# Kernel optimization log

Measured on AMD Instinct MI355X. Metric: run time of the kernel, lower is better.

The kernel has to match this reference:

```python
import jax, jax.numpy as jnp
import numpy as np

B, D = 65536, 365

def _linp(k, fan_in, fan_out):
    # torch nn.Linear default init: U(-1/sqrt(fan_in), 1/sqrt(fan_in))
    kw, kb = jax.random.split(k)
    bound = 1.0 / np.sqrt(fan_in)
    W = jax.random.uniform(kw, (fan_in, fan_out), jnp.float32, -bound, bound)
    b = jax.random.uniform(kb, (fan_out,), jnp.float32, -bound, bound)
    return W, b

def setup_inputs() -> dict:
    key = jax.random.key(0)
    ks = jax.random.split(key, 9)
    x = jax.random.normal(ks[0], (B, D), jnp.float32)
    W1, b1 = _linp(ks[1], D, 512)
    W2, b2 = _linp(ks[2], 512, 256)
    W3, b3 = _linp(ks[3], 256, 128)
    Ws, bs = _linp(ks[4], 6, 32)
    Wc1, bc1 = _linp(ks[5], 128 + 32, 64)
    Wc2, bc2 = _linp(ks[6], 64, 32)
    Wc3, bc3 = _linp(ks[7], 32, 1)
    return dict(x=x, W1=W1, b1=b1, W2=W2, b2=b2, W3=W3, b3=b3,
                Ws=Ws, bs=bs, Wc1=Wc1, bc1=bc1, Wc2=Wc2, bc2=bc2,
                Wc3=Wc3, bc3=bc3)

def _row_stats(x):
    # fused row-wise moments: mean, std (ddof=1), min, max, skew, kurtosis
    mu = jnp.mean(x, axis=1, keepdims=True)          # [B,1]
    c = x - mu                                        # [B,D]
    var1 = jnp.sum(c * c, axis=1) / (x.shape[1] - 1)  # unbiased, matches torch.std()
    sigma = jnp.sqrt(var1)
    m3 = jnp.mean(c ** 3, axis=1)
    m4 = jnp.mean(c ** 4, axis=1)
    skew = m3 / (sigma ** 3 + 1e-8)
    kurt = m4 / (sigma ** 4 + 1e-8)
    return jnp.stack([mu[:, 0], sigma, jnp.min(x, axis=1), jnp.max(x, axis=1), skew, kurt], axis=1)

def reference(x, W1, b1, W2, b2, W3, b3, Ws, bs, Wc1, bc1, Wc2, bc2, Wc3, bc3):
    h = jax.nn.relu(x @ W1 + b1)
    h = jax.nn.relu(h @ W2 + b2)
    seq = jax.nn.relu(h @ W3 + b3)            # [B,128]
    stat = _row_stats(x) @ Ws + bs            # [B,32]
    comb = jnp.concatenate([seq, stat], axis=1)
    c = jax.nn.relu(comb @ Wc1 + bc1)
    c = jax.nn.relu(c @ Wc2 + bc2)
    out = jax.nn.sigmoid(c @ Wc3 + bc3)       # [B,1]
    return out[:, 0]
```

## Files before the change

### kernel.cpp

```cpp
#include <hip/hip_runtime.h>
#include <math.h>

typedef __attribute__((ext_vector_type(8)))  short short8;
typedef __attribute__((ext_vector_type(16))) float float16;

#define DEVI __device__ __forceinline__

DEVI short f2bf(float f) {
    unsigned u = __float_as_uint(f);
    u = (u + 0x7fffu + ((u >> 16) & 1u)) >> 16;
    return (short)u;
}
DEVI unsigned pk2(float a, float b) {
    return (unsigned)(unsigned short)f2bf(a) | ((unsigned)(unsigned short)f2bf(b) << 16);
}
DEVI float16 mfma16(short8 a, short8 b, float16 c) {
    return __builtin_amdgcn_mfma_f32_32x32x16_bf16(a, b, c, 0, 0, 0);
}
DEVI int rowof(int r, int h) { return (r & 3) + 8 * (r >> 2) + 4 * h; }
DEVI short8 lds8(const short* p) { return *(const short8*)p; }

#define W1T_OFF  0
#define W2T_OFF  188416
#define W3T_OFF  319488
#define WC1T_OFF 352256
#define WC2T_OFF 362496

__global__ void prep_v2(const float* __restrict__ W1, const float* __restrict__ W2,
                        const float* __restrict__ W3, const float* __restrict__ Wc1,
                        const float* __restrict__ Wc2, short* __restrict__ ws) {
    __shared__ short T[16 * 72];
    int b = blockIdx.x, t = threadIdx.x;
    const float* src; int K, N; size_t base; int kc, nb;
    if (b < 184)        {            src = W1;  K = 365; N = 512; base = W1T_OFF;  kc = b >> 3;  nb = b & 7; }
    else if (b < 312)   { int l = b - 184; src = W2;  K = 512; N = 256; base = W2T_OFF;  kc = l >> 2;  nb = l & 3; }
    else if (b < 344)   { int l = b - 312; src = W3;  K = 256; N = 128; base = W3T_OFF;  kc = l >> 1;  nb = l & 1; }
    else if (b < 354)   {            src = Wc1; K = 160; N = 64;  base = WC1T_OFF; kc = b - 344; nb = 0; }
    else                {            src = Wc2; K = 64;  N = 32;  base = WC2T_OFF; kc = b - 354; nb = 0; }
    int n = nb * 64 + (t & 63);
    int kr = t >> 6;
    #pragma unroll
    for (int i = 0; i < 4; ++i) {
        int krow = kr + 4 * i;
        int k = kc * 16 + krow;
        float v = (k < K && n < N) ? src[(size_t)k * N + n] : 0.f;
        T[krow * 72 + (t & 63)] = f2bf(v);
    }
    __syncthreads();
    int n2 = t >> 2, ksq = (t & 3) * 4;
    int ng = nb * 64 + n2;
    if (ng < N) {
        unsigned lo = (unsigned)(unsigned short)T[ksq * 72 + n2]
                    | ((unsigned)(unsigned short)T[(ksq + 1) * 72 + n2] << 16);
        unsigned hi = (unsigned)(unsigned short)T[(ksq + 2) * 72 + n2]
                    | ((unsigned)(unsigned short)T[(ksq + 3) * 72 + n2] << 16);
        uint2 d; d.x = lo; d.y = hi;
        *(uint2*)(ws + base + ((size_t)kc * N + ng) * 16 + ksq) = d;
    }
}

__global__ __launch_bounds__(512, 4)
void fused_v2(const float* __restrict__ x,
              const float* __restrict__ b1f, const float* __restrict__ b2f,
              const float* __restrict__ b3f, const float* __restrict__ Wsf,
              const float* __restrict__ bsf, const float* __restrict__ bc1f,
              const float* __restrict__ bc2f, const float* __restrict__ Wc3f,
              const float* __restrict__ bc3f,
              const short* __restrict__ wsw, float* __restrict__ out)
{
    __shared__ __align__(16) char smem[65536];
    short* XT    = (short*)smem;
    short* SB    = (short*)(smem + 48128);
    short* C1    = (short*)smem;
    short* FEATL = (short*)(smem + 12288);
    float* C2    = (float*)(smem + 20480);

    const short* W1t  = wsw + W1T_OFF;
    const short* W2t  = wsw + W2T_OFF;
    const short* W3t  = wsw + W3T_OFF;
    const short* Wc1t = wsw + WC1T_OFF;
    const short* Wc2t = wsw + WC2T_OFF;

    const int tid  = (int)threadIdx.x;
    const int lane = tid & 63;
    const int wv   = tid >> 6;
    const int m    = lane & 31;
    const int h    = lane >> 5;
    const int mt   = wv & 1;
    const int nl   = wv >> 1;
    const int rowBase = (int)blockIdx.x * 64;

    const int r0 = tid >> 3, j0 = tid & 7;
    const float* xrow = x + (size_t)(rowBase + r0) * 365;
    float s1 = 0.f, s2 = 0.f, s3 = 0.f, s4 = 0.f, mn = 1e30f, mx = -1e30f;
    #pragma unroll
    for (int i = 0; i < 6; ++i) {
        int o = j0 + 8 * i;
        if (o <= 45) {
            float xf[8];
            #pragma unroll
            for (int jj = 0; jj < 8; ++jj) {
                int col = o * 8 + jj;
                xf[jj] = (col < 365) ? xrow[col] : 0.f;
            }
            #pragma unroll
            for (int jj = 0; jj < 8; ++jj) {
                int col = o * 8 + jj;
                if (col < 365) {
                    float v = xf[jj], v2 = v * v;
                    s1 += v; s2 += v2; s3 += v2 * v; s4 += v2 * v2;
                    mn = fminf(mn, v); mx = fmaxf(mx, v);
                }
            }
            int4 w4;
            w4.x = (int)pk2(xf[0], xf[1]); w4.y = (int)pk2(xf[2], xf[3]);
            w4.z = (int)pk2(xf[4], xf[5]); w4.w = (int)pk2(xf[6], xf[7]);
            *(int4*)(XT + r0 * 376 + o * 8) = w4;
        }
    }
    #pragma unroll
    for (int off = 1; off <= 4; off <<= 1) {
        s1 += __shfl_xor(s1, off); s2 += __shfl_xor(s2, off);
        s3 += __shfl_xor(s3, off); s4 += __shfl_xor(s4, off);
        mn = fminf(mn, __shfl_xor(mn, off)); mx = fmaxf(mx, __shfl_xor(mx, off));
    }
    unsigned fdw0, fdw1;
    {
        float mean  = s1 * (1.0f / 365.0f);
        float var1  = (s2 - 365.0f * mean * mean) * (1.0f / 364.0f);
        float sigma = sqrtf(var1);
        float m3 = (s3 - 3.0f * mean * s2) * (1.0f / 365.0f) + 2.0f * mean * mean * mean;
        float mm = mean * mean;
        float m4 = (s4 - 4.0f * mean * s3 + 6.0f * mm * s2) * (1.0f / 365.0f) - 3.0f * mm * mm;
        float sg2 = sigma * sigma;
        float skew = m3 / (sigma * sg2 + 1e-8f);
        float kurt = m4 / (sg2 * sg2 + 1e-8f);
        float st[6] = { mean, sigma, mn, mx, skew, kurt };
        float f[4];
        #pragma unroll
        for (int c0 = 0; c0 < 4; ++c0) {
            int c = 4 * j0 + c0;
            float acc = bsf[c];
            #pragma unroll
            for (int jj = 0; jj < 6; ++jj) acc += st[jj] * Wsf[jj * 32 + c];
            f[c0] = acc;
        }
        fdw0 = pk2(f[0], f[1]); fdw1 = pk2(f[2], f[3]);
    }
    __syncthreads();

    float16 h2a0, h2a1;
    #pragma unroll
    for (int i = 0; i < 16; ++i) { h2a0[i] = 0.f; h2a1[i] = 0.f; }

    const short* Ap = XT + (mt * 32 + m) * 376 + h * 8;

    for (int p = 0; p < 2; ++p) {
        float16 ga0, ga1;
        #pragma unroll
        for (int i = 0; i < 16; ++i) { ga0[i] = 0.f; ga1[i] = 0.f; }
        int nc0 = 256 * p + 32 * nl;
        const short* Bp0 = W1t + (nc0 + m) * 16 + h * 8;
        const short* Bp1 = Bp0 + 128 * 16;
        #pragma unroll
        for (int kc = 0; kc < 23; ++kc) {
            short8 a  = lds8(Ap + kc * 16);
            short8 b0 = *(const short8*)(Bp0 + kc * 8192);
            short8 b1 = *(const short8*)(Bp1 + kc * 8192);
            ga0 = mfma16(a, b0, ga0);
            ga1 = mfma16(a, b1, ga1);
        }
        #pragma unroll
        for (int q = 0; q < 2; ++q) {
            __syncthreads();
            {
                int nc = 256 * p + 128 * q + 32 * nl;
                float bb = b1f[nc + m];
                float16 A;
                if (q) A = ga1; else A = ga0;
                #pragma unroll
                for (int r = 0; r < 16; ++r) {
                    int rw = mt * 32 + rowof(r, h);
                    SB[rw * 136 + 32 * nl + m] = f2bf(fmaxf(A[r] + bb, 0.f));
                }
            }
            __syncthreads();
            int slab = 2 * p + q;
            const short* A2p  = SB + (mt * 32 + m) * 136 + h * 8;
            const short* B2p0 = W2t + (size_t)slab * 8 * 4096 + (32 * nl + m) * 16 + h * 8;
            const short* B2p1 = B2p0 + 128 * 16;
            #pragma unroll
            for (int i = 0; i < 8; ++i) {
                short8 a  = lds8(A2p + i * 16);
                short8 b0 = *(const short8*)(B2p0 + i * 4096);
                short8 b1 = *(const short8*)(B2p1 + i * 4096);
                h2a0 = mfma16(a, b0, h2a0);
                h2a1 = mfma16(a, b1, h2a1);
            }
        }
    }

    float16 g3a;
    #pragma unroll
    for (int i = 0; i < 16; ++i) g3a[i] = 0.f;
    for (int s = 0; s < 2; ++s) {
        __syncthreads();
        {
            float bb = b2f[32 * nl + 128 * s + m];
            float16 A;
            if (s) A = h2a1; else A = h2a0;
            #pragma unroll
            for (int r = 0; r < 16; ++r) {
                int rw = mt * 32 + rowof(r, h);
                SB[rw * 136 + 32 * nl + m] = f2bf(fmaxf(A[r] + bb, 0.f));
            }
        }
        __syncthreads();
        const short* A3p = SB + (mt * 32 + m) * 136 + h * 8;
        const short* B3p = W3t + (size_t)s * 8 * 2048 + (32 * nl + m) * 16 + h * 8;
        #pragma unroll
        for (int i = 0; i < 8; ++i) {
            short8 a = lds8(A3p + i * 16);
            short8 b = *(const short8*)(B3p + i * 2048);
            g3a = mfma16(a, b, g3a);
        }
    }

    __syncthreads();
    {
        float bb = b3f[32 * nl + m];
        #pragma unroll
        for (int r = 0; r < 16; ++r) {
            int rw = mt * 32 + rowof(r, h);
            SB[rw * 136 + 32 * nl + m] = f2bf(fmaxf(g3a[r] + bb, 0.f));
        }
        *(unsigned*)(FEATL + r0 * 40 + 4 * j0)     = fdw0;
        *(unsigned*)(FEATL + r0 * 40 + 4 * j0 + 2) = fdw1;
    }
    __syncthreads();

    if (wv < 4) {
        int nt4 = wv >> 1;
        float16 g4a;
        #pragma unroll
        for (int i = 0; i < 16; ++i) g4a[i] = 0.f;
        const short* A4p = SB + (mt * 32 + m) * 136 + h * 8;
        const short* B4p = Wc1t + (32 * nt4 + m) * 16 + h * 8;
        #pragma unroll
        for (int i = 0; i < 8; ++i) {
            short8 a = lds8(A4p + i * 16);
            short8 b = *(const short8*)(B4p + i * 1024);
            g4a = mfma16(a, b, g4a);
        }
        const short* AF = FEATL + (mt * 32 + m) * 40 + h * 8;
        #pragma unroll
        for (int i = 0; i < 2; ++i) {
            short8 a = lds8(AF + i * 16);
            short8 b = *(const short8*)(B4p + (8 + i) * 1024);
            g4a = mfma16(a, b, g4a);
        }
        float bb = bc1f[32 * nt4 + m];
        #pragma unroll
        for (int r = 0; r < 16; ++r) {
            int rw = mt * 32 + rowof(r, h);
            C1[rw * 72 + 32 * nt4 + m] = f2bf(fmaxf(g4a[r] + bb, 0.f));
        }
    }
    __syncthreads();

    if (wv < 2) {
        float16 g5;
        #pragma unroll
        for (int i = 0; i < 16; ++i) g5[i] = 0.f;
        const short* A5p = C1 + (wv * 32 + m) * 72 + h * 8;
        const short* B5p = Wc2t + m * 16 + h * 8;
        #pragma unroll
        for (int i = 0; i < 4; ++i) {
            short8 a = lds8(A5p + i * 16);
            short8 b = *(const short8*)(B5p + i * 512);
            g5 = mfma16(a, b, g5);
        }
        float bb = bc2f[m];
        #pragma unroll
        for (int r = 0; r < 16; ++r) {
            int rw = wv * 32 + rowof(r, h);
            C2[rw * 33 + m] = fmaxf(g5[r] + bb, 0.f);
        }
    }
    __syncthreads();

    if (tid < 64) {
        float z = bc3f[0];
        #pragma unroll
        for (int i = 0; i < 32; ++i) z += C2[tid * 33 + i] * Wc3f[i];
        out[rowBase + tid] = 1.0f / (1.0f + expf(-z));
    }
}

extern "C" void kernel_launch(void* const* d_in, const int* in_sizes, int n_in,
                              void* d_out, int out_size, void* d_ws, size_t ws_size,
                              hipStream_t stream)
{
    (void)in_sizes; (void)n_in; (void)out_size; (void)ws_size;
    const float* x   = (const float*)d_in[0];
    const float* W1  = (const float*)d_in[1];
    const float* b1  = (const float*)d_in[2];
    const float* W2  = (const float*)d_in[3];
    const float* b2  = (const float*)d_in[4];
    const float* W3  = (const float*)d_in[5];
    const float* b3  = (const float*)d_in[6];
    const float* Ws  = (const float*)d_in[7];
    const float* bs  = (const float*)d_in[8];
    const float* Wc1 = (const float*)d_in[9];
    const float* bc1 = (const float*)d_in[10];
    const float* Wc2 = (const float*)d_in[11];
    const float* bc2 = (const float*)d_in[12];
    const float* Wc3 = (const float*)d_in[13];
    const float* bc3 = (const float*)d_in[14];
    short* ws = (short*)d_ws;

    prep_v2<<<358, 256, 0, stream>>>(W1, W2, W3, Wc1, Wc2, ws);
    fused_v2<<<1024, 512, 0, stream>>>(x, b1, b2, b3, Ws, bs, bc1, bc2, Wc3, bc3,
                                       ws, (float*)d_out);
}
```

Measured before the change: 237.5 us.

## Software-prefetch weight fragments through register ring buffers and restructure layer-1 loop

Weight B-fragments for every MLP layer are now loaded from global memory a few steps ahead into small register ring buffers, so global load latency overlaps with MFMA work instead of stalling each iteration. The layer-1 loop is reorganized into four 128-wide column passes with one accumulator each, interleaving layer-2 accumulation after every pass. Biases are hoisted into registers at kernel start, and x loads and output stores use nontemporal hints. The added prefetch registers may raise register pressure and risk occupancy loss under the 512x4 launch bounds.

```diff
diff --git a/kernel.cpp b/kernel.cpp
--- a/kernel.cpp
+++ b/kernel.cpp
@@ -19,6 +19,7 @@
 }
 DEVI int rowof(int r, int h) { return (r & 3) + 8 * (r >> 2) + 4 * h; }
 DEVI short8 lds8(const short* p) { return *(const short8*)p; }
+DEVI short8 gld8(const short* p) { return *(const short8*)p; }
 
 #define W1T_OFF  0
 #define W2T_OFF  188416
@@ -60,7 +61,7 @@
 }
 
 __global__ __launch_bounds__(512, 4)
-void fused_v2(const float* __restrict__ x,
+void fused_v3(const float* __restrict__ x,
               const float* __restrict__ b1f, const float* __restrict__ b2f,
               const float* __restrict__ b3f, const float* __restrict__ Wsf,
               const float* __restrict__ bsf, const float* __restrict__ bc1f,
@@ -87,8 +88,22 @@
     const int m    = lane & 31;
     const int h    = lane >> 5;
     const int mt   = wv & 1;
-    const int nl   = wv >> 1;
+    const int nc   = wv >> 1;
     const int rowBase = (int)blockIdx.x * 64;
+
+    const short* B1b  = W1t + (nc * 32 + m) * 16 + h * 8;
+    const short* B2b0 = W2t + (nc * 32 + m) * 16 + h * 8;
+    const short* B2b1 = B2b0 + 128 * 16;
+    short8 rb[4], rc0[2], rc1[2];
+    #pragma unroll
+    for (int i = 0; i < 4; ++i) rb[i] = gld8(B1b + i * 8192);
+    #pragma unroll
+    for (int i = 0; i < 2; ++i) { rc0[i] = gld8(B2b0 + i * 4096); rc1[i] = gld8(B2b1 + i * 4096); }
+    float bb1[4];
+    #pragma unroll
+    for (int p = 0; p < 4; ++p) bb1[p] = b1f[p * 128 + nc * 32 + m];
+    float bb2a = b2f[nc * 32 + m], bb2b = b2f[128 + nc * 32 + m];
+    float bb3 = b3f[nc * 32 + m];
 
     const int r0 = tid >> 3, j0 = tid & 7;
     const float* xrow = x + (size_t)(rowBase + r0) * 365;
@@ -101,7 +116,7 @@
             #pragma unroll
             for (int jj = 0; jj < 8; ++jj) {
                 int col = o * 8 + jj;
-                xf[jj] = (col < 365) ? xrow[col] : 0.f;
+                xf[jj] = (col < 365) ? __builtin_nontemporal_load(xrow + col) : 0.f;
             }
             #pragma unroll
             for (int jj = 0; jj < 8; ++jj) {
@@ -152,88 +167,83 @@
     float16 h2a0, h2a1;
     #pragma unroll
     for (int i = 0; i < 16; ++i) { h2a0[i] = 0.f; h2a1[i] = 0.f; }
-
-    const short* Ap = XT + (mt * 32 + m) * 376 + h * 8;
-
-    for (int p = 0; p < 2; ++p) {
-        float16 ga0, ga1;
-        #pragma unroll
-        for (int i = 0; i < 16; ++i) { ga0[i] = 0.f; ga1[i] = 0.f; }
-        int nc0 = 256 * p + 32 * nl;
-        const short* Bp0 = W1t + (nc0 + m) * 16 + h * 8;
-        const short* Bp1 = Bp0 + 128 * 16;
+    const short* Ap  = XT + (mt * 32 + m) * 376 + h * 8;
+    const short* A2p = SB + (mt * 32 + m) * 136 + h * 8;
+
+    #pragma unroll
+    for (int p = 0; p < 4; ++p) {
+        float16 ga;
+        #pragma unroll
+        for (int i = 0; i < 16; ++i) ga[i] = 0.f;
         #pragma unroll
         for (int kc = 0; kc < 23; ++kc) {
-            short8 a  = lds8(Ap + kc * 16);
-            short8 b0 = *(const short8*)(Bp0 + kc * 8192);
-            short8 b1 = *(const short8*)(Bp1 + kc * 8192);
-            ga0 = mfma16(a, b0, ga0);
-            ga1 = mfma16(a, b1, ga1);
-        }
-        #pragma unroll
-        for (int q = 0; q < 2; ++q) {
-            __syncthreads();
-            {
-                int nc = 256 * p + 128 * q + 32 * nl;
-                float bb = b1f[nc + m];
-                float16 A;
-                if (q) A = ga1; else A = ga0;
-                #pragma unroll
-                for (int r = 0; r < 16; ++r) {
-                    int rw = mt * 32 + rowof(r, h);
-                    SB[rw * 136 + 32 * nl + m] = f2bf(fmaxf(A[r] + bb, 0.f));
-                }
+            int t = p * 23 + kc;
+            short8 b = rb[t & 3];
+            int tn = t + 4;
+            if (tn < 92) {
+                int pp = tn / 23, kk = tn - pp * 23;
+                rb[tn & 3] = gld8(B1b + pp * 2048 + kk * 8192);
             }
-            __syncthreads();
-            int slab = 2 * p + q;
-            const short* A2p  = SB + (mt * 32 + m) * 136 + h * 8;
-            const short* B2p0 = W2t + (size_t)slab * 8 * 4096 + (32 * nl + m) * 16 + h * 8;
-            const short* B2p1 = B2p0 + 128 * 16;
-            #pragma unroll
-            for (int i = 0; i < 8; ++i) {
-                short8 a  = lds8(A2p + i * 16);
-                short8 b0 = *(const short8*)(B2p0 + i * 4096);
-                short8 b1 = *(const short8*)(B2p1 + i * 4096);
-                h2a0 = mfma16(a, b0, h2a0);
-                h2a1 = mfma16(a, b1, h2a1);
+            short8 a = lds8(Ap + kc * 16);
+            ga = mfma16(a, b, ga);
+        }
+        __syncthreads();
+        {
+            float bb = bb1[p];
+            #pragma unroll
+            for (int r = 0; r < 16; ++r)
+                SB[(mt * 32 + rowof(r, h)) * 136 + nc * 32 + m] = f2bf(fmaxf(ga[r] + bb, 0.f));
+        }
+        __syncthreads();
+        #pragma unroll
+        for (int i = 0; i < 8; ++i) {
+            int t2 = p * 8 + i;
+            short8 b0 = rc0[t2 & 1], b1 = rc1[t2 & 1];
+            int tn = t2 + 2;
+            if (tn < 32) {
+                rc0[tn & 1] = gld8(B2b0 + tn * 4096);
+                rc1[tn & 1] = gld8(B2b1 + tn * 4096);
             }
-        }
-    }
-
+            short8 a = lds8(A2p + i * 16);
+            h2a0 = mfma16(a, b0, h2a0);
+            h2a1 = mfma16(a, b1, h2a1);
+        }
+    }
+
+    const short* B3b = W3t + (nc * 32 + m) * 16 + h * 8;
+    short8 rd[2];
+    rd[0] = gld8(B3b);
+    rd[1] = gld8(B3b + 2048);
     float16 g3a;
     #pragma unroll
     for (int i = 0; i < 16; ++i) g3a[i] = 0.f;
+    #pragma unroll
     for (int s = 0; s < 2; ++s) {
         __syncthreads();
         {
-            float bb = b2f[32 * nl + 128 * s + m];
-            float16 A;
-            if (s) A = h2a1; else A = h2a0;
-            #pragma unroll
-            for (int r = 0; r < 16; ++r) {
-                int rw = mt * 32 + rowof(r, h);
-                SB[rw * 136 + 32 * nl + m] = f2bf(fmaxf(A[r] + bb, 0.f));
-            }
+            float bb = s ? bb2b : bb2a;
+            float16 H = s ? h2a1 : h2a0;
+            #pragma unroll
+            for (int r = 0; r < 16; ++r)
+                SB[(mt * 32 + rowof(r, h)) * 136 + nc * 32 + m] = f2bf(fmaxf(H[r] + bb, 0.f));
         }
         __syncthreads();
-        const short* A3p = SB + (mt * 32 + m) * 136 + h * 8;
-        const short* B3p = W3t + (size_t)s * 8 * 2048 + (32 * nl + m) * 16 + h * 8;
         #pragma unroll
         for (int i = 0; i < 8; ++i) {
-            short8 a = lds8(A3p + i * 16);
-            short8 b = *(const short8*)(B3p + i * 2048);
+            int t3 = s * 8 + i;
+            short8 b = rd[t3 & 1];
+            int tn = t3 + 2;
+            if (tn < 16) rd[tn & 1] = gld8(B3b + tn * 2048);
+            short8 a = lds8(A2p + i * 16);
             g3a = mfma16(a, b, g3a);
         }
     }
 
     __syncthreads();
     {
-        float bb = b3f[32 * nl + m];
-        #pragma unroll
-        for (int r = 0; r < 16; ++r) {
-            int rw = mt * 32 + rowof(r, h);
-            SB[rw * 136 + 32 * nl + m] = f2bf(fmaxf(g3a[r] + bb, 0.f));
-        }
+        #pragma unroll
+        for (int r = 0; r < 16; ++r)
+            SB[(mt * 32 + rowof(r, h)) * 136 + nc * 32 + m] = f2bf(fmaxf(g3a[r] + bb3, 0.f));
         *(unsigned*)(FEATL + r0 * 40 + 4 * j0)     = fdw0;
         *(unsigned*)(FEATL + r0 * 40 + 4 * j0 + 2) = fdw1;
     }
@@ -241,23 +251,23 @@
 
     if (wv < 4) {
         int nt4 = wv >> 1;
+        const short* B4b = Wc1t + (32 * nt4 + m) * 16 + h * 8;
+        short8 wB[10];
+        #pragma unroll
+        for (int i = 0; i < 10; ++i) wB[i] = gld8(B4b + i * 1024);
         float16 g4a;
         #pragma unroll
         for (int i = 0; i < 16; ++i) g4a[i] = 0.f;
-        const short* A4p = SB + (mt * 32 + m) * 136 + h * 8;
-        const short* B4p = Wc1t + (32 * nt4 + m) * 16 + h * 8;
         #pragma unroll
         for (int i = 0; i < 8; ++i) {
-            short8 a = lds8(A4p + i * 16);
-            short8 b = *(const short8*)(B4p + i * 1024);
-            g4a = mfma16(a, b, g4a);
+            short8 a = lds8(A2p + i * 16);
+            g4a = mfma16(a, wB[i], g4a);
         }
         const short* AF = FEATL + (mt * 32 + m) * 40 + h * 8;
         #pragma unroll
         for (int i = 0; i < 2; ++i) {
             short8 a = lds8(AF + i * 16);
-            short8 b = *(const short8*)(B4p + (8 + i) * 1024);
-            g4a = mfma16(a, b, g4a);
+            g4a = mfma16(a, wB[8 + i], g4a);
         }
         float bb = bc1f[32 * nt4 + m];
         #pragma unroll
@@ -269,16 +279,18 @@
     __syncthreads();
 
     if (wv < 2) {
+        const short* B5b = Wc2t + m * 16 + h * 8;
+        short8 wB[4];
+        #pragma unroll
+        for (int i = 0; i < 4; ++i) wB[i] = gld8(B5b + i * 512);
         float16 g5;
         #pragma unroll
         for (int i = 0; i < 16; ++i) g5[i] = 0.f;
         const short* A5p = C1 + (wv * 32 + m) * 72 + h * 8;
-        const short* B5p = Wc2t + m * 16 + h * 8;
         #pragma unroll
         for (int i = 0; i < 4; ++i) {
             short8 a = lds8(A5p + i * 16);
-            short8 b = *(const short8*)(B5p + i * 512);
-            g5 = mfma16(a, b, g5);
+            g5 = mfma16(a, wB[i], g5);
         }
         float bb = bc2f[m];
         #pragma unroll
@@ -293,7 +305,7 @@
         float z = bc3f[0];
         #pragma unroll
         for (int i = 0; i < 32; ++i) z += C2[tid * 33 + i] * Wc3f[i];
-        out[rowBase + tid] = 1.0f / (1.0f + expf(-z));
+        __builtin_nontemporal_store(1.0f / (1.0f + expf(-z)), &out[rowBase + tid]);
     }
 }
 
@@ -320,6 +332,6 @@
     short* ws = (short*)d_ws;
 
     prep_v2<<<358, 256, 0, stream>>>(W1, W2, W3, Wc1, Wc2, ws);
-    fused_v2<<<1024, 512, 0, stream>>>(x, b1, b2, b3, Ws, bs, bc1, bc2, Wc3, bc3,
+    fused_v3<<<1024, 512, 0, stream>>>(x, b1, b2, b3, Ws, bs, bc1, bc2, Wc3, bc3,
                                        ws, (float*)d_out);
 }
```

Result: slower. 271.2 us (+14.2%).

## Remap waves so each owns a column tile across both row halves, sharing weight loads

Applied to the files above, without the earlier changes.

Changes the wave-to-tile mapping in the three big GEMM stages. Each of the 8 waves now computes one 32-column weight tile for both 32-row halves, instead of two column tiles for one row half. Each global weight fragment is therefore loaded once and feeds two MFMAs, which halves global/L2 weight traffic per block, while LDS activation reads double. Bias loads are hoisted to the kernel start, and the writebacks of intermediate activations are split across wave halves between barriers.

```diff
diff --git a/kernel.cpp b/kernel.cpp
--- a/kernel.cpp
+++ b/kernel.cpp
@@ -19,6 +19,7 @@
 }
 DEVI int rowof(int r, int h) { return (r & 3) + 8 * (r >> 2) + 4 * h; }
 DEVI short8 lds8(const short* p) { return *(const short8*)p; }
+DEVI short8 gld8(const short* p) { return *(const short8*)p; }
 
 #define W1T_OFF  0
 #define W2T_OFF  188416
@@ -60,7 +61,7 @@
 }
 
 __global__ __launch_bounds__(512, 4)
-void fused_v2(const float* __restrict__ x,
+void fused_v4(const float* __restrict__ x,
               const float* __restrict__ b1f, const float* __restrict__ b2f,
               const float* __restrict__ b3f, const float* __restrict__ Wsf,
               const float* __restrict__ bsf, const float* __restrict__ bc1f,
@@ -86,9 +87,12 @@
     const int wv   = tid >> 6;
     const int m    = lane & 31;
     const int h    = lane >> 5;
-    const int mt   = wv & 1;
-    const int nl   = wv >> 1;
     const int rowBase = (int)blockIdx.x * 64;
+
+    float bb1a = b1f[32 * wv + m];
+    float bb1b = b1f[256 + 32 * wv + m];
+    float bb2  = b2f[32 * wv + m];
+    float bb3  = b3f[32 * (wv & 3) + m];
 
     const int r0 = tid >> 3, j0 = tid & 7;
     const float* xrow = x + (size_t)(rowBase + r0) * 365;
@@ -149,143 +153,133 @@
     }
     __syncthreads();
 
-    float16 h2a0, h2a1;
-    #pragma unroll
-    for (int i = 0; i < 16; ++i) { h2a0[i] = 0.f; h2a1[i] = 0.f; }
-
-    const short* Ap = XT + (mt * 32 + m) * 376 + h * 8;
-
+    float16 ha0, ha1;
+    #pragma unroll
+    for (int i = 0; i < 16; ++i) { ha0[i] = 0.f; ha1[i] = 0.f; }
+
+    const short* Ap0  = XT + m * 376 + h * 8;
+    const short* Ap1  = XT + (32 + m) * 376 + h * 8;
+    const short* A2p0 = SB + m * 136 + h * 8;
+    const short* A2p1 = SB + (32 + m) * 136 + h * 8;
+    const int stcol = 32 * (wv & 3) + m;
+
+    #pragma unroll
     for (int p = 0; p < 2; ++p) {
         float16 ga0, ga1;
         #pragma unroll
         for (int i = 0; i < 16; ++i) { ga0[i] = 0.f; ga1[i] = 0.f; }
-        int nc0 = 256 * p + 32 * nl;
-        const short* Bp0 = W1t + (nc0 + m) * 16 + h * 8;
-        const short* Bp1 = Bp0 + 128 * 16;
+        const short* B1 = W1t + (256 * p + 32 * wv + m) * 16 + h * 8;
         #pragma unroll
         for (int kc = 0; kc < 23; ++kc) {
-            short8 a  = lds8(Ap + kc * 16);
-            short8 b0 = *(const short8*)(Bp0 + kc * 8192);
-            short8 b1 = *(const short8*)(Bp1 + kc * 8192);
-            ga0 = mfma16(a, b0, ga0);
-            ga1 = mfma16(a, b1, ga1);
-        }
-        #pragma unroll
-        for (int q = 0; q < 2; ++q) {
+            short8 b  = gld8(B1 + kc * 8192);
+            short8 a0 = lds8(Ap0 + kc * 16);
+            short8 a1 = lds8(Ap1 + kc * 16);
+            ga0 = mfma16(a0, b, ga0);
+            ga1 = mfma16(a1, b, ga1);
+        }
+        float bb = p ? bb1b : bb1a;
+        #pragma unroll
+        for (int s = 0; s < 2; ++s) {
+            int sl = 2 * p + s;
             __syncthreads();
-            {
-                int nc = 256 * p + 128 * q + 32 * nl;
-                float bb = b1f[nc + m];
-                float16 A;
-                if (q) A = ga1; else A = ga0;
+            if ((wv >> 2) == s) {
                 #pragma unroll
                 for (int r = 0; r < 16; ++r) {
-                    int rw = mt * 32 + rowof(r, h);
-                    SB[rw * 136 + 32 * nl + m] = f2bf(fmaxf(A[r] + bb, 0.f));
+                    SB[rowof(r, h) * 136 + stcol]        = f2bf(fmaxf(ga0[r] + bb, 0.f));
+                    SB[(32 + rowof(r, h)) * 136 + stcol] = f2bf(fmaxf(ga1[r] + bb, 0.f));
                 }
             }
             __syncthreads();
-            int slab = 2 * p + q;
-            const short* A2p  = SB + (mt * 32 + m) * 136 + h * 8;
-            const short* B2p0 = W2t + (size_t)slab * 8 * 4096 + (32 * nl + m) * 16 + h * 8;
-            const short* B2p1 = B2p0 + 128 * 16;
+            const short* B2 = W2t + sl * 8 * 4096 + (32 * wv + m) * 16 + h * 8;
             #pragma unroll
             for (int i = 0; i < 8; ++i) {
-                short8 a  = lds8(A2p + i * 16);
-                short8 b0 = *(const short8*)(B2p0 + i * 4096);
-                short8 b1 = *(const short8*)(B2p1 + i * 4096);
-                h2a0 = mfma16(a, b0, h2a0);
-                h2a1 = mfma16(a, b1, h2a1);
-            }
-        }
-    }
-
-    float16 g3a;
-    #pragma unroll
-    for (int i = 0; i < 16; ++i) g3a[i] = 0.f;
-    for (int s = 0; s < 2; ++s) {
+                short8 b  = gld8(B2 + i * 4096);
+                short8 a0 = lds8(A2p0 + i * 16);
+                short8 a1 = lds8(A2p1 + i * 16);
+                ha0 = mfma16(a0, b, ha0);
+                ha1 = mfma16(a1, b, ha1);
+            }
+        }
+    }
+
+    float16 g3;
+    #pragma unroll
+    for (int i = 0; i < 16; ++i) g3[i] = 0.f;
+    const short* A3p = SB + ((wv >> 2) * 32 + m) * 136 + h * 8;
+    #pragma unroll
+    for (int t = 0; t < 2; ++t) {
         __syncthreads();
-        {
-            float bb = b2f[32 * nl + 128 * s + m];
-            float16 A;
-            if (s) A = h2a1; else A = h2a0;
+        if ((wv >> 2) == t) {
             #pragma unroll
             for (int r = 0; r < 16; ++r) {
-                int rw = mt * 32 + rowof(r, h);
-                SB[rw * 136 + 32 * nl + m] = f2bf(fmaxf(A[r] + bb, 0.f));
+                SB[rowof(r, h) * 136 + stcol]        = f2bf(fmaxf(ha0[r] + bb2, 0.f));
+                SB[(32 + rowof(r, h)) * 136 + stcol] = f2bf(fmaxf(ha1[r] + bb2, 0.f));
             }
         }
         __syncthreads();
-        const short* A3p = SB + (mt * 32 + m) * 136 + h * 8;
-        const short* B3p = W3t + (size_t)s * 8 * 2048 + (32 * nl + m) * 16 + h * 8;
+        const short* B3 = W3t + t * 8 * 2048 + (32 * (wv & 3) + m) * 16 + h * 8;
         #pragma unroll
         for (int i = 0; i < 8; ++i) {
+            short8 b = gld8(B3 + i * 2048);
             short8 a = lds8(A3p + i * 16);
-            short8 b = *(const short8*)(B3p + i * 2048);
-            g3a = mfma16(a, b, g3a);
+            g3 = mfma16(a, b, g3);
         }
     }
 
     __syncthreads();
     {
-        float bb = b3f[32 * nl + m];
-        #pragma unroll
-        for (int r = 0; r < 16; ++r) {
-            int rw = mt * 32 + rowof(r, h);
-            SB[rw * 136 + 32 * nl + m] = f2bf(fmaxf(g3a[r] + bb, 0.f));
-        }
+        int rb = (wv >> 2) * 32;
+        #pragma unroll
+        for (int r = 0; r < 16; ++r)
+            SB[(rb + rowof(r, h)) * 136 + stcol] = f2bf(fmaxf(g3[r] + bb3, 0.f));
         *(unsigned*)(FEATL + r0 * 40 + 4 * j0)     = fdw0;
         *(unsigned*)(FEATL + r0 * 40 + 4 * j0 + 2) = fdw1;
     }
     __syncthreads();
 
     if (wv < 4) {
-        int nt4 = wv >> 1;
-        float16 g4a;
-        #pragma unroll
-        for (int i = 0; i < 16; ++i) g4a[i] = 0.f;
-        const short* A4p = SB + (mt * 32 + m) * 136 + h * 8;
-        const short* B4p = Wc1t + (32 * nt4 + m) * 16 + h * 8;
+        int m4 = wv & 1, c4 = wv >> 1;
+        const short* B4 = Wc1t + (32 * c4 + m) * 16 + h * 8;
+        const short* A4 = SB + (m4 * 32 + m) * 136 + h * 8;
+        float16 g4;
+        #pragma unroll
+        for (int i = 0; i < 16; ++i) g4[i] = 0.f;
         #pragma unroll
         for (int i = 0; i < 8; ++i) {
-            short8 a = lds8(A4p + i * 16);
-            short8 b = *(const short8*)(B4p + i * 1024);
-            g4a = mfma16(a, b, g4a);
-        }
-        const short* AF = FEATL + (mt * 32 + m) * 40 + h * 8;
+            short8 b = gld8(B4 + i * 1024);
+            short8 a = lds8(A4 + i * 16);
+            g4 = mfma16(a, b, g4);
+        }
+        const short* AF = FEATL + (m4 * 32 + m) * 40 + h * 8;
         #pragma unroll
         for (int i = 0; i < 2; ++i) {
+            short8 b = gld8(B4 + (8 + i) * 1024);
             short8 a = lds8(AF + i * 16);
-            short8 b = *(const short8*)(B4p + (8 + i) * 1024);
-            g4a = mfma16(a, b, g4a);
-        }
-        float bb = bc1f[32 * nt4 + m];
-        #pragma unroll
-        for (int r = 0; r < 16; ++r) {
-            int rw = mt * 32 + rowof(r, h);
-            C1[rw * 72 + 32 * nt4 + m] = f2bf(fmaxf(g4a[r] + bb, 0.f));
-        }
+            g4 = mfma16(a, b, g4);
+        }
+        float bb = bc1f[32 * c4 + m];
+        #pragma unroll
+        for (int r = 0; r < 16; ++r)
+            C1[(m4 * 32 + rowof(r, h)) * 72 + 32 * c4 + m] = f2bf(fmaxf(g4[r] + bb, 0.f));
     }
     __syncthreads();
 
     if (wv < 2) {
+        const short* B5 = Wc2t + m * 16 + h * 8;
+        const short* A5 = C1 + (wv * 32 + m) * 72 + h * 8;
         float16 g5;
         #pragma unroll
         for (int i = 0; i < 16; ++i) g5[i] = 0.f;
-        const short* A5p = C1 + (wv * 32 + m) * 72 + h * 8;
-        const short* B5p = Wc2t + m * 16 + h * 8;
         #pragma unroll
         for (int i = 0; i < 4; ++i) {
-            short8 a = lds8(A5p + i * 16);
-            short8 b = *(const short8*)(B5p + i * 512);
+            short8 b = gld8(B5 + i * 512);
+            short8 a = lds8(A5 + i * 16);
             g5 = mfma16(a, b, g5);
         }
         float bb = bc2f[m];
         #pragma unroll
-        for (int r = 0; r < 16; ++r) {
-            int rw = wv * 32 + rowof(r, h);
-            C2[rw * 33 + m] = fmaxf(g5[r] + bb, 0.f);
-        }
+        for (int r = 0; r < 16; ++r)
+            C2[(wv * 32 + rowof(r, h)) * 33 + m] = fmaxf(g5[r] + bb, 0.f);
     }
     __syncthreads();
 
@@ -320,6 +314,6 @@
     short* ws = (short*)d_ws;
 
     prep_v2<<<358, 256, 0, stream>>>(W1, W2, W3, Wc1, Wc2, ws);
-    fused_v2<<<1024, 512, 0, stream>>>(x, b1, b2, b3, Ws, bs, bc1, bc2, Wc3, bc3,
+    fused_v4<<<1024, 512, 0, stream>>>(x, b1, b2, b3, Ws, bs, bc1, bc2, Wc3, bc3,
                                        ws, (float*)d_out);
 }
```

Result: no change. 236.6 us (-0.4%).
